# Optimization experiments

Measured on AMD Instinct MI355X. Metric: run time of the kernel, lower is better.

The kernel has to match this reference:

```python
import jax, jax.numpy as jnp
import numpy as np

B, L, D, H, HD = 4, 1024, 768, 12, 64

def setup_inputs() -> dict:
    key = jax.random.key(0)
    ks = jax.random.split(key, 8)
    s = 0.02
    return {
        "x": jax.random.normal(ks[0], (B, L, D), dtype=jnp.float32),
        "Wq": jax.random.normal(ks[1], (D, H * HD), dtype=jnp.float32) * s,
        "Wk": jax.random.normal(ks[2], (D, H * HD), dtype=jnp.float32) * s,
        "Wv": jax.random.normal(ks[3], (D, H * HD), dtype=jnp.float32) * s,
        "pre_attn": jax.random.normal(ks[4], (H, H), dtype=jnp.float32),
        "post_attn": jax.random.normal(ks[5], (H, H), dtype=jnp.float32),
        "Wo": jax.random.normal(ks[6], (H * HD, D), dtype=jnp.float32) * s,
        "bo": jnp.zeros((D,), dtype=jnp.float32),
    }

def reference(x, Wq, Wk, Wv, pre_attn, post_attn, Wo, bo):
    b, l, _ = x.shape
    # projections (no bias)
    q = x @ Wq  # [B, L, H*HD]
    k = x @ Wk
    v = x @ Wv
    # split heads: b l (h d) -> b h l d
    split = lambda t: t.reshape(b, l, H, HD).transpose(0, 2, 1, 3)
    qh, kh, vh = split(q), split(k), split(v)
    scale = 1.0 / jnp.sqrt(jnp.float32(HD))
    a = jnp.einsum('bhid,bhjd->bhij', qh, kh) * scale  # [B,H,L,L]
    # talking-heads: pre-softmax mix, softmax, post-softmax mix
    a = jnp.einsum('bhij,hg->bgij', a, pre_attn)
    a = jax.nn.softmax(a, axis=-1)
    a = jnp.einsum('bhij,hg->bgij', a, post_attn)
    av = jnp.einsum('bhij,bhjd->bhid', a, vh)  # [B,H,L,HD]
    # faithful to original: raw reshape of [(b h), l, d] -> [b, l, h*d]
    # (row-major, mixes h and l axes exactly like torch .reshape)
    av = av.reshape(b, l, H * HD)
    return av @ Wo + bo
```

## Files before the change

### kernel.cpp

```cpp
#include <hip/hip_runtime.h>

#define D_MODEL 768
#define NHEAD   12
#define HDIM    64
#define SEQ     1024
#define BATCH   4
#define QBLK    16
#define KVBLK   32

typedef __attribute__((ext_vector_type(8))) short short8v;
typedef __attribute__((ext_vector_type(4))) float f32x4;

__device__ __forceinline__ ushort f2bf(float f) {
    union { float f; unsigned u; } c; c.f = f;
    unsigned r = c.u + 0x7fffu + ((c.u >> 16) & 1u);
    return (ushort)(r >> 16);
}

__global__ void cast_bf16_kernel(const float* __restrict__ src,
                                 ushort* __restrict__ dst, int n4)
{
    int idx = blockIdx.x * blockDim.x + threadIdx.x;
    if (idx >= n4) return;
    float4 v = ((const float4*)src)[idx];
    ushort4 o;
    o.x = f2bf(v.x); o.y = f2bf(v.y); o.z = f2bf(v.z); o.w = f2bf(v.w);
    ((ushort4*)dst)[idx] = o;
}

__global__ __launch_bounds__(256) void castT_kernel(const float* __restrict__ W,
                                                    ushort* __restrict__ WT)
{
    __shared__ float tile[32][33];
    const int kb  = blockIdx.x * 32;
    const int nb  = blockIdx.y * 32;
    const int tid = threadIdx.x;
    const int r   = tid >> 3;
    const int c4  = (tid & 7) * 4;

    float4 v = *(const float4*)(W + (size_t)(kb + r) * 768 + nb + c4);
    tile[r][c4 + 0] = v.x; tile[r][c4 + 1] = v.y;
    tile[r][c4 + 2] = v.z; tile[r][c4 + 3] = v.w;
    __syncthreads();

    ushort4 o;
    o.x = f2bf(tile[c4 + 0][r]);
    o.y = f2bf(tile[c4 + 1][r]);
    o.z = f2bf(tile[c4 + 2][r]);
    o.w = f2bf(tile[c4 + 3][r]);
    *(ushort4*)(WT + (size_t)(nb + r) * 768 + kb + c4) = o;
}

__global__ __launch_bounds__(256) void vT_kernel(const ushort* __restrict__ vbf,
                                                 ushort* __restrict__ vt)
{
    __shared__ ushort tile[32][33];
    const int j0 = blockIdx.x * 32;
    const int d0 = blockIdx.y * 32;
    const int bh = blockIdx.z;
    const int b  = bh / NHEAD, h = bh % NHEAD;
    const int tid = threadIdx.x;
    const int r   = tid >> 3;
    const int c4  = (tid & 7) * 4;

    ushort4 v = *(const ushort4*)(vbf + ((size_t)b * SEQ + j0 + r) * D_MODEL + h * HDIM + d0 + c4);
    tile[r][c4 + 0] = v.x; tile[r][c4 + 1] = v.y;
    tile[r][c4 + 2] = v.z; tile[r][c4 + 3] = v.w;
    __syncthreads();

    ushort4 o;
    o.x = tile[c4 + 0][r]; o.y = tile[c4 + 1][r];
    o.z = tile[c4 + 2][r]; o.w = tile[c4 + 3][r];
    *(ushort4*)(vt + ((size_t)bh * HDIM + d0 + r) * SEQ + j0 + c4) = o;
}

template<int BF16OUT>
__global__ __launch_bounds__(256) void gemm_bf16_kernel(
    const ushort* __restrict__ A, const ushort* __restrict__ BT,
    void* __restrict__ C0v, void* __restrict__ C1v, void* __restrict__ C2v,
    const float* __restrict__ bias)
{
    __shared__ __align__(16) ushort As[128 * 32];
    __shared__ __align__(16) ushort Bs[128 * 32];

    const int bm  = blockIdx.x * 128;
    const int bnG = blockIdx.y * 128;
    const int sel = bnG / 768;
    void* Cv = (sel == 0) ? C0v : ((sel == 1) ? C1v : C2v);
    const int ncol0 = bnG - sel * 768;

    const int tid  = threadIdx.x;
    const int lane = tid & 63;
    const int wave = tid >> 6;
    const int wm = wave >> 1, wn = wave & 1;

    f32x4 acc[4][4];
    #pragma unroll
    for (int i = 0; i < 4; i++)
        #pragma unroll
        for (int j = 0; j < 4; j++)
            acc[i][j] = (f32x4){0.f, 0.f, 0.f, 0.f};

    const int sr = tid >> 2;
    const int sk = (tid & 3) * 8;
    const ushort* Ap = A  + (size_t)(bm  + sr) * 768 + sk;
    const ushort* Bp = BT + (size_t)(bnG + sr) * 768 + sk;
    char* AsDst = (char*)As + tid * 16;
    char* BsDst = (char*)Bs + tid * 16;

    for (int k0 = 0; k0 < 768; k0 += 32) {
        __syncthreads();
        __builtin_amdgcn_global_load_lds(
            (const __attribute__((address_space(1))) void*)(Ap + k0),
            (__attribute__((address_space(3))) void*)AsDst, 16, 0, 0);
        __builtin_amdgcn_global_load_lds(
            (const __attribute__((address_space(1))) void*)(Ap + (size_t)64 * 768 + k0),
            (__attribute__((address_space(3))) void*)(AsDst + 4096), 16, 0, 0);
        __builtin_amdgcn_global_load_lds(
            (const __attribute__((address_space(1))) void*)(Bp + k0),
            (__attribute__((address_space(3))) void*)BsDst, 16, 0, 0);
        __builtin_amdgcn_global_load_lds(
            (const __attribute__((address_space(1))) void*)(Bp + (size_t)64 * 768 + k0),
            (__attribute__((address_space(3))) void*)(BsDst + 4096), 16, 0, 0);
        __syncthreads();

        short8v a[4], b[4];
        #pragma unroll
        for (int i = 0; i < 4; i++)
            a[i] = *(const short8v*)((const char*)As +
                     (wm * 64 + i * 16 + (lane & 15)) * 64 + (lane >> 4) * 16);
        #pragma unroll
        for (int j = 0; j < 4; j++)
            b[j] = *(const short8v*)((const char*)Bs +
                     (wn * 64 + j * 16 + (lane & 15)) * 64 + (lane >> 4) * 16);
        #pragma unroll
        for (int i = 0; i < 4; i++)
            #pragma unroll
            for (int j = 0; j < 4; j++)
                acc[i][j] = __builtin_amdgcn_mfma_f32_16x16x32_bf16(a[i], b[j], acc[i][j], 0, 0, 0);
    }

    const int cc = lane & 15, cr = lane >> 4;
    #pragma unroll
    for (int j = 0; j < 4; j++) {
        const int col = ncol0 + wn * 64 + j * 16 + cc;
        const float badd = bias ? bias[col] : 0.f;
        #pragma unroll
        for (int i = 0; i < 4; i++) {
            #pragma unroll
            for (int r = 0; r < 4; r++) {
                const int row = bm + wm * 64 + i * 16 + cr * 4 + r;
                if (BF16OUT)
                    ((ushort*)Cv)[(size_t)row * 768 + col] = f2bf(acc[i][j][r] + badd);
                else
                    ((float*)Cv)[(size_t)row * 768 + col] = acc[i][j][r] + badd;
            }
        }
    }
}

__global__ __launch_bounds__(768, 1) void attn_mfma_kernel(
    const ushort* __restrict__ qb, const ushort* __restrict__ kb,
    const ushort* __restrict__ vt, const float* __restrict__ pre_attn,
    const float* __restrict__ post_attn, ushort* __restrict__ avb)
{
    __shared__ __align__(16) float s_raw[NHEAD][QBLK][36];
    __shared__ float pre_l[NHEAD * NHEAD];
    __shared__ float post_l[NHEAD * NHEAD];
    __shared__ float l_lds[NHEAD][QBLK];

    const int i0  = blockIdx.x * QBLK;
    const int b   = blockIdx.y;
    const int tid = threadIdx.x;
    const int lane = tid & 63;
    const int h    = tid >> 6;

    if (tid < 144) pre_l[tid] = pre_attn[tid] * 0.125f;
    else if (tid < 288) post_l[tid - 144] = post_attn[tid - 144];

    const int lr = lane & 15;
    const int lc = lane >> 4;

    const ushort* qbase = qb + ((size_t)b * SEQ + i0 + lr) * D_MODEL + h * HDIM + lc * 8;
    const short8v a_q0 = *(const short8v*)(qbase);
    const short8v a_q1 = *(const short8v*)(qbase + 32);

    const ushort* kbase  = kb + ((size_t)b * SEQ + lr) * D_MODEL + h * HDIM + lc * 8;
    const ushort* vtbase = vt + (((size_t)b * NHEAD + h) * HDIM + lr) * SEQ + lc * 8;

    float lsum = 0.f;
    for (int j0 = 0; j0 < SEQ; j0 += KVBLK) {
        f32x4 s_frag[2];
        #pragma unroll
        for (int cf = 0; cf < 2; cf++) {
            short8v bk0 = *(const short8v*)(kbase + (size_t)(j0 + cf * 16) * D_MODEL);
            short8v bk1 = *(const short8v*)(kbase + (size_t)(j0 + cf * 16) * D_MODEL + 32);
            f32x4 acc = (f32x4){0.f, 0.f, 0.f, 0.f};
            acc = __builtin_amdgcn_mfma_f32_16x16x32_bf16(a_q0, bk0, acc, 0, 0, 0);
            acc = __builtin_amdgcn_mfma_f32_16x16x32_bf16(a_q1, bk1, acc, 0, 0, 0);
            s_frag[cf] = acc;
        }
        __syncthreads();
        #pragma unroll
        for (int cf = 0; cf < 2; cf++)
            #pragma unroll
            for (int rr = 0; rr < 4; rr++)
                s_raw[h][lc * 4 + rr][cf * 16 + lr] = s_frag[cf][rr];
        __syncthreads();

        float mix[8];
        #pragma unroll
        for (int c = 0; c < 8; c++) mix[c] = 0.f;
        #pragma unroll
        for (int hh = 0; hh < NHEAD; hh++) {
            const float w = pre_l[hh * NHEAD + h];
            const float4 s0 = *(const float4*)(&s_raw[hh][lr][lc * 8]);
            const float4 s1 = *(const float4*)(&s_raw[hh][lr][lc * 8 + 4]);
            mix[0] = fmaf(s0.x, w, mix[0]); mix[1] = fmaf(s0.y, w, mix[1]);
            mix[2] = fmaf(s0.z, w, mix[2]); mix[3] = fmaf(s0.w, w, mix[3]);
            mix[4] = fmaf(s1.x, w, mix[4]); mix[5] = fmaf(s1.y, w, mix[5]);
            mix[6] = fmaf(s1.z, w, mix[6]); mix[7] = fmaf(s1.w, w, mix[7]);
        }
        #pragma unroll
        for (int c = 0; c < 8; c++) lsum += __expf(mix[c]);
    }
    float lrow = lsum;
    lrow += __shfl_xor(lrow, 16);
    lrow += __shfl_xor(lrow, 32);
    if (lc == 0) l_lds[h][lr] = lrow;
    __syncthreads();

    float il[NHEAD];
    #pragma unroll
    for (int hh = 0; hh < NHEAD; hh++) il[hh] = 1.f / l_lds[hh][lr];

    f32x4 o_acc[4];
    #pragma unroll
    for (int d = 0; d < 4; d++) o_acc[d] = (f32x4){0.f, 0.f, 0.f, 0.f};

    for (int j0 = 0; j0 < SEQ; j0 += KVBLK) {
        f32x4 s_frag[2];
        #pragma unroll
        for (int cf = 0; cf < 2; cf++) {
            short8v bk0 = *(const short8v*)(kbase + (size_t)(j0 + cf * 16) * D_MODEL);
            short8v bk1 = *(const short8v*)(kbase + (size_t)(j0 + cf * 16) * D_MODEL + 32);
            f32x4 acc = (f32x4){0.f, 0.f, 0.f, 0.f};
            acc = __builtin_amdgcn_mfma_f32_16x16x32_bf16(a_q0, bk0, acc, 0, 0, 0);
            acc = __builtin_amdgcn_mfma_f32_16x16x32_bf16(a_q1, bk1, acc, 0, 0, 0);
            s_frag[cf] = acc;
        }
        __syncthreads();
        #pragma unroll
        for (int cf = 0; cf < 2; cf++)
            #pragma unroll
            for (int rr = 0; rr < 4; rr++)
                s_raw[h][lc * 4 + rr][cf * 16 + lr] = s_frag[cf][rr];
        __syncthreads();

        float mix[8];
        #pragma unroll
        for (int c = 0; c < 8; c++) mix[c] = 0.f;
        #pragma unroll
        for (int hh = 0; hh < NHEAD; hh++) {
            const float w = pre_l[hh * NHEAD + h];
            const float4 s0 = *(const float4*)(&s_raw[hh][lr][lc * 8]);
            const float4 s1 = *(const float4*)(&s_raw[hh][lr][lc * 8 + 4]);
            mix[0] = fmaf(s0.x, w, mix[0]); mix[1] = fmaf(s0.y, w, mix[1]);
            mix[2] = fmaf(s0.z, w, mix[2]); mix[3] = fmaf(s0.w, w, mix[3]);
            mix[4] = fmaf(s1.x, w, mix[4]); mix[5] = fmaf(s1.y, w, mix[5]);
            mix[6] = fmaf(s1.z, w, mix[6]); mix[7] = fmaf(s1.w, w, mix[7]);
        }
        float e[8];
        #pragma unroll
        for (int c = 0; c < 8; c++) e[c] = __expf(mix[c]);

        __syncthreads();
        #pragma unroll
        for (int c = 0; c < 8; c += 4)
            *(float4*)(&s_raw[h][lr][lc * 8 + c]) = *(float4*)(&e[c]);
        __syncthreads();

        float pmix[8];
        #pragma unroll
        for (int c = 0; c < 8; c++) pmix[c] = 0.f;
        #pragma unroll
        for (int hh = 0; hh < NHEAD; hh++) {
            const float w = post_l[hh * NHEAD + h] * il[hh];
            const float4 e0 = *(const float4*)(&s_raw[hh][lr][lc * 8]);
            const float4 e1 = *(const float4*)(&s_raw[hh][lr][lc * 8 + 4]);
            pmix[0] = fmaf(e0.x, w, pmix[0]); pmix[1] = fmaf(e0.y, w, pmix[1]);
            pmix[2] = fmaf(e0.z, w, pmix[2]); pmix[3] = fmaf(e0.w, w, pmix[3]);
            pmix[4] = fmaf(e1.x, w, pmix[4]); pmix[5] = fmaf(e1.y, w, pmix[5]);
            pmix[6] = fmaf(e1.z, w, pmix[6]); pmix[7] = fmaf(e1.w, w, pmix[7]);
        }
        short8v pa;
        #pragma unroll
        for (int c = 0; c < 8; c++) ((ushort*)&pa)[c] = f2bf(pmix[c]);

        #pragma unroll
        for (int d = 0; d < 4; d++) {
            short8v bv = *(const short8v*)(vtbase + (size_t)(d * 16) * SEQ + j0);
            o_acc[d] = __builtin_amdgcn_mfma_f32_16x16x32_bf16(pa, bv, o_acc[d], 0, 0, 0);
        }
    }

    #pragma unroll
    for (int d = 0; d < 4; d++)
        #pragma unroll
        for (int rr = 0; rr < 4; rr++)
            avb[(((size_t)b * NHEAD + h) * SEQ + i0 + lc * 4 + rr) * HDIM + d * 16 + lr]
                = f2bf(o_acc[d][rr]);
}

extern "C" void kernel_launch(void* const* d_in, const int* in_sizes, int n_in,
                              void* d_out, int out_size, void* d_ws, size_t ws_size,
                              hipStream_t stream)
{
    const float* x    = (const float*)d_in[0];
    const float* Wq   = (const float*)d_in[1];
    const float* Wk   = (const float*)d_in[2];
    const float* Wv   = (const float*)d_in[3];
    const float* pre  = (const float*)d_in[4];
    const float* post = (const float*)d_in[5];
    const float* Wo   = (const float*)d_in[6];
    const float* bo   = (const float*)d_in[7];
    float* out = (float*)d_out;

    const size_t SZ = (size_t)BATCH * SEQ * D_MODEL;
    ushort* qbf    = (ushort*)d_ws;
    ushort* kbf    = qbf + SZ;
    ushort* vbf    = kbf + SZ;
    ushort* vt     = vbf + SZ;
    ushort* xb_avb = vt  + SZ;
    ushort* qkvT   = xb_avb + SZ;
    ushort* WoT    = qkvT + (size_t)2304 * 768;

    cast_bf16_kernel<<<(int)(SZ / 4 + 255) / 256, 256, 0, stream>>>(x, xb_avb, (int)(SZ / 4));
    castT_kernel<<<dim3(24, 24), 256, 0, stream>>>(Wq, qkvT);
    castT_kernel<<<dim3(24, 24), 256, 0, stream>>>(Wk, qkvT + (size_t)768 * 768);
    castT_kernel<<<dim3(24, 24), 256, 0, stream>>>(Wv, qkvT + (size_t)2 * 768 * 768);
    castT_kernel<<<dim3(24, 24), 256, 0, stream>>>(Wo, WoT);

    gemm_bf16_kernel<1><<<dim3(32, 18), 256, 0, stream>>>(xb_avb, qkvT, qbf, kbf, vbf, nullptr);

    vT_kernel<<<dim3(32, 2, BATCH * NHEAD), 256, 0, stream>>>(vbf, vt);

    attn_mfma_kernel<<<dim3(SEQ / QBLK, BATCH), 768, 0, stream>>>(qbf, kbf, vt, pre, post, xb_avb);

    gemm_bf16_kernel<0><<<dim3(32, 6), 256, 0, stream>>>(qbf == nullptr ? nullptr : xb_avb, WoT, out, out, out, bo);
}
```

Baseline: 355.1 us.

## Fuse V transpose into QKV GEMM, merge weight casts, double KV tile and buffers

The QKV GEMM epilogue now writes V directly in transposed per-head layout, which removes the separate vT kernel and the vbf buffer. The four weight cast-transpose launches are merged into one 3D-grid launch. In the attention kernel the KV block grows from 32 to 64 and the LDS score buffers are split or double-buffered, cutting __syncthreads per tile from four to one or two. exp is replaced by exp2 with log2e folded into the pre-mix weights. The cost is more LDS and registers per block, and the scattered ushort4 V-transpose stores may not coalesce well.

```diff
diff --git a/kernel.cpp b/kernel.cpp
--- a/kernel.cpp
+++ b/kernel.cpp
@@ -6,7 +6,8 @@
 #define SEQ     1024
 #define BATCH   4
 #define QBLK    16
-#define KVBLK   32
+#define KVBLK   64
+#define NT      (SEQ / KVBLK)
 
 typedef __attribute__((ext_vector_type(8))) short short8v;
 typedef __attribute__((ext_vector_type(4))) float f32x4;
@@ -28,10 +29,17 @@
     ((ushort4*)dst)[idx] = o;
 }
 
-__global__ __launch_bounds__(256) void castT_kernel(const float* __restrict__ W,
-                                                    ushort* __restrict__ WT)
+__global__ __launch_bounds__(256) void castT4_kernel(
+    const float* __restrict__ W0, const float* __restrict__ W1,
+    const float* __restrict__ W2, const float* __restrict__ W3,
+    ushort* __restrict__ D0, ushort* __restrict__ D1,
+    ushort* __restrict__ D2, ushort* __restrict__ D3)
 {
     __shared__ float tile[32][33];
+    const int z = blockIdx.z;
+    const float* W = (z == 0) ? W0 : (z == 1) ? W1 : (z == 2) ? W2 : W3;
+    ushort*     D = (z == 0) ? D0 : (z == 1) ? D1 : (z == 2) ? D2 : D3;
+
     const int kb  = blockIdx.x * 32;
     const int nb  = blockIdx.y * 32;
     const int tid = threadIdx.x;
@@ -48,37 +56,14 @@
     o.y = f2bf(tile[c4 + 1][r]);
     o.z = f2bf(tile[c4 + 2][r]);
     o.w = f2bf(tile[c4 + 3][r]);
-    *(ushort4*)(WT + (size_t)(nb + r) * 768 + kb + c4) = o;
-}
-
-__global__ __launch_bounds__(256) void vT_kernel(const ushort* __restrict__ vbf,
-                                                 ushort* __restrict__ vt)
-{
-    __shared__ ushort tile[32][33];
-    const int j0 = blockIdx.x * 32;
-    const int d0 = blockIdx.y * 32;
-    const int bh = blockIdx.z;
-    const int b  = bh / NHEAD, h = bh % NHEAD;
-    const int tid = threadIdx.x;
-    const int r   = tid >> 3;
-    const int c4  = (tid & 7) * 4;
-
-    ushort4 v = *(const ushort4*)(vbf + ((size_t)b * SEQ + j0 + r) * D_MODEL + h * HDIM + d0 + c4);
-    tile[r][c4 + 0] = v.x; tile[r][c4 + 1] = v.y;
-    tile[r][c4 + 2] = v.z; tile[r][c4 + 3] = v.w;
-    __syncthreads();
-
-    ushort4 o;
-    o.x = tile[c4 + 0][r]; o.y = tile[c4 + 1][r];
-    o.z = tile[c4 + 2][r]; o.w = tile[c4 + 3][r];
-    *(ushort4*)(vt + ((size_t)bh * HDIM + d0 + r) * SEQ + j0 + c4) = o;
+    *(ushort4*)(D + (size_t)(nb + r) * 768 + kb + c4) = o;
 }
 
 template<int BF16OUT>
 __global__ __launch_bounds__(256) void gemm_bf16_kernel(
     const ushort* __restrict__ A, const ushort* __restrict__ BT,
     void* __restrict__ C0v, void* __restrict__ C1v, void* __restrict__ C2v,
-    const float* __restrict__ bias)
+    const float* __restrict__ bias, ushort* __restrict__ VT)
 {
     __shared__ __align__(16) ushort As[128 * 32];
     __shared__ __align__(16) ushort Bs[128 * 32];
@@ -141,6 +126,23 @@
     }
 
     const int cc = lane & 15, cr = lane >> 4;
+    if (BF16OUT && VT != nullptr && sel == 2) {
+        #pragma unroll
+        for (int j = 0; j < 4; j++) {
+            const int hcol = ncol0 + wn * 64 + j * 16 + cc;
+            const int h2 = hcol >> 6, dd = hcol & 63;
+            #pragma unroll
+            for (int i = 0; i < 4; i++) {
+                const int row0 = bm + wm * 64 + i * 16 + cr * 4;
+                const int bb = row0 >> 10, jj = row0 & 1023;
+                ushort4 o;
+                o.x = f2bf(acc[i][j][0]); o.y = f2bf(acc[i][j][1]);
+                o.z = f2bf(acc[i][j][2]); o.w = f2bf(acc[i][j][3]);
+                *(ushort4*)(VT + (((size_t)bb * NHEAD + h2) * HDIM + dd) * SEQ + jj) = o;
+            }
+        }
+        return;
+    }
     #pragma unroll
     for (int j = 0; j < 4; j++) {
         const int col = ncol0 + wn * 64 + j * 16 + cc;
@@ -164,7 +166,8 @@
     const ushort* __restrict__ vt, const float* __restrict__ pre_attn,
     const float* __restrict__ post_attn, ushort* __restrict__ avb)
 {
-    __shared__ __align__(16) float s_raw[NHEAD][QBLK][36];
+    __shared__ __align__(16) float sA[NHEAD][QBLK][68];
+    __shared__ __align__(16) float sE[NHEAD][QBLK][68];
     __shared__ float pre_l[NHEAD * NHEAD];
     __shared__ float post_l[NHEAD * NHEAD];
     __shared__ float l_lds[NHEAD][QBLK];
@@ -175,7 +178,7 @@
     const int lane = tid & 63;
     const int h    = tid >> 6;
 
-    if (tid < 144) pre_l[tid] = pre_attn[tid] * 0.125f;
+    if (tid < 144) pre_l[tid] = pre_attn[tid] * (0.125f * 1.44269504f);
     else if (tid < 288) post_l[tid - 144] = post_attn[tid - 144];
 
     const int lr = lane & 15;
@@ -189,40 +192,50 @@
     const ushort* vtbase = vt + (((size_t)b * NHEAD + h) * HDIM + lr) * SEQ + lc * 8;
 
     float lsum = 0.f;
-    for (int j0 = 0; j0 < SEQ; j0 += KVBLK) {
-        f32x4 s_frag[2];
-        #pragma unroll
-        for (int cf = 0; cf < 2; cf++) {
-            short8v bk0 = *(const short8v*)(kbase + (size_t)(j0 + cf * 16) * D_MODEL);
-            short8v bk1 = *(const short8v*)(kbase + (size_t)(j0 + cf * 16) * D_MODEL + 32);
-            f32x4 acc = (f32x4){0.f, 0.f, 0.f, 0.f};
-            acc = __builtin_amdgcn_mfma_f32_16x16x32_bf16(a_q0, bk0, acc, 0, 0, 0);
-            acc = __builtin_amdgcn_mfma_f32_16x16x32_bf16(a_q1, bk1, acc, 0, 0, 0);
-            s_frag[cf] = acc;
-        }
-        __syncthreads();
-        #pragma unroll
-        for (int cf = 0; cf < 2; cf++)
+    for (int t = 0; t < NT; t++) {
+        const int j0 = t * KVBLK;
+        float (*S)[QBLK][68] = (t & 1) ? sE : sA;
+
+        f32x4 sf[4];
+        #pragma unroll
+        for (int cf = 0; cf < 4; cf++) {
+            const ushort* kp = kbase + (size_t)(j0 + cf * 16) * D_MODEL;
+            short8v bk0 = *(const short8v*)(kp);
+            short8v bk1 = *(const short8v*)(kp + 32);
+            f32x4 a = (f32x4){0.f, 0.f, 0.f, 0.f};
+            a = __builtin_amdgcn_mfma_f32_16x16x32_bf16(a_q0, bk0, a, 0, 0, 0);
+            a = __builtin_amdgcn_mfma_f32_16x16x32_bf16(a_q1, bk1, a, 0, 0, 0);
+            sf[cf] = a;
+        }
+        #pragma unroll
+        for (int cf = 0; cf < 4; cf++)
             #pragma unroll
             for (int rr = 0; rr < 4; rr++)
-                s_raw[h][lc * 4 + rr][cf * 16 + lr] = s_frag[cf][rr];
-        __syncthreads();
-
-        float mix[8];
-        #pragma unroll
-        for (int c = 0; c < 8; c++) mix[c] = 0.f;
+                S[h][lc * 4 + rr][cf * 16 + lr] = sf[cf][rr];
+        __syncthreads();
+
+        float mix[16];
+        #pragma unroll
+        for (int c = 0; c < 16; c++) mix[c] = 0.f;
         #pragma unroll
         for (int hh = 0; hh < NHEAD; hh++) {
             const float w = pre_l[hh * NHEAD + h];
-            const float4 s0 = *(const float4*)(&s_raw[hh][lr][lc * 8]);
-            const float4 s1 = *(const float4*)(&s_raw[hh][lr][lc * 8 + 4]);
-            mix[0] = fmaf(s0.x, w, mix[0]); mix[1] = fmaf(s0.y, w, mix[1]);
-            mix[2] = fmaf(s0.z, w, mix[2]); mix[3] = fmaf(s0.w, w, mix[3]);
-            mix[4] = fmaf(s1.x, w, mix[4]); mix[5] = fmaf(s1.y, w, mix[5]);
-            mix[6] = fmaf(s1.z, w, mix[6]); mix[7] = fmaf(s1.w, w, mix[7]);
-        }
-        #pragma unroll
-        for (int c = 0; c < 8; c++) lsum += __expf(mix[c]);
+            const float* row = &S[hh][lr][0];
+            const float4 a0 = *(const float4*)(row + lc * 8);
+            const float4 a1 = *(const float4*)(row + lc * 8 + 4);
+            const float4 a2 = *(const float4*)(row + 32 + lc * 8);
+            const float4 a3 = *(const float4*)(row + 36 + lc * 8);
+            mix[0]  = fmaf(a0.x, w, mix[0]);  mix[1]  = fmaf(a0.y, w, mix[1]);
+            mix[2]  = fmaf(a0.z, w, mix[2]);  mix[3]  = fmaf(a0.w, w, mix[3]);
+            mix[4]  = fmaf(a1.x, w, mix[4]);  mix[5]  = fmaf(a1.y, w, mix[5]);
+            mix[6]  = fmaf(a1.z, w, mix[6]);  mix[7]  = fmaf(a1.w, w, mix[7]);
+            mix[8]  = fmaf(a2.x, w, mix[8]);  mix[9]  = fmaf(a2.y, w, mix[9]);
+            mix[10] = fmaf(a2.z, w, mix[10]); mix[11] = fmaf(a2.w, w, mix[11]);
+            mix[12] = fmaf(a3.x, w, mix[12]); mix[13] = fmaf(a3.y, w, mix[13]);
+            mix[14] = fmaf(a3.z, w, mix[14]); mix[15] = fmaf(a3.w, w, mix[15]);
+        }
+        #pragma unroll
+        for (int c = 0; c < 16; c++) lsum += exp2f(mix[c]);
     }
     float lrow = lsum;
     lrow += __shfl_xor(lrow, 16);
@@ -238,69 +251,93 @@
     #pragma unroll
     for (int d = 0; d < 4; d++) o_acc[d] = (f32x4){0.f, 0.f, 0.f, 0.f};
 
-    for (int j0 = 0; j0 < SEQ; j0 += KVBLK) {
-        f32x4 s_frag[2];
-        #pragma unroll
-        for (int cf = 0; cf < 2; cf++) {
-            short8v bk0 = *(const short8v*)(kbase + (size_t)(j0 + cf * 16) * D_MODEL);
-            short8v bk1 = *(const short8v*)(kbase + (size_t)(j0 + cf * 16) * D_MODEL + 32);
-            f32x4 acc = (f32x4){0.f, 0.f, 0.f, 0.f};
-            acc = __builtin_amdgcn_mfma_f32_16x16x32_bf16(a_q0, bk0, acc, 0, 0, 0);
-            acc = __builtin_amdgcn_mfma_f32_16x16x32_bf16(a_q1, bk1, acc, 0, 0, 0);
-            s_frag[cf] = acc;
-        }
-        __syncthreads();
-        #pragma unroll
-        for (int cf = 0; cf < 2; cf++)
+    for (int t = 0; t < NT; t++) {
+        const int j0 = t * KVBLK;
+
+        f32x4 sf[4];
+        #pragma unroll
+        for (int cf = 0; cf < 4; cf++) {
+            const ushort* kp = kbase + (size_t)(j0 + cf * 16) * D_MODEL;
+            short8v bk0 = *(const short8v*)(kp);
+            short8v bk1 = *(const short8v*)(kp + 32);
+            f32x4 a = (f32x4){0.f, 0.f, 0.f, 0.f};
+            a = __builtin_amdgcn_mfma_f32_16x16x32_bf16(a_q0, bk0, a, 0, 0, 0);
+            a = __builtin_amdgcn_mfma_f32_16x16x32_bf16(a_q1, bk1, a, 0, 0, 0);
+            sf[cf] = a;
+        }
+        #pragma unroll
+        for (int cf = 0; cf < 4; cf++)
             #pragma unroll
             for (int rr = 0; rr < 4; rr++)
-                s_raw[h][lc * 4 + rr][cf * 16 + lr] = s_frag[cf][rr];
-        __syncthreads();
-
-        float mix[8];
-        #pragma unroll
-        for (int c = 0; c < 8; c++) mix[c] = 0.f;
+                sA[h][lc * 4 + rr][cf * 16 + lr] = sf[cf][rr];
+        __syncthreads();
+
+        float mix[16];
+        #pragma unroll
+        for (int c = 0; c < 16; c++) mix[c] = 0.f;
         #pragma unroll
         for (int hh = 0; hh < NHEAD; hh++) {
             const float w = pre_l[hh * NHEAD + h];
-            const float4 s0 = *(const float4*)(&s_raw[hh][lr][lc * 8]);
-            const float4 s1 = *(const float4*)(&s_raw[hh][lr][lc * 8 + 4]);
-            mix[0] = fmaf(s0.x, w, mix[0]); mix[1] = fmaf(s0.y, w, mix[1]);
-            mix[2] = fmaf(s0.z, w, mix[2]); mix[3] = fmaf(s0.w, w, mix[3]);
-            mix[4] = fmaf(s1.x, w, mix[4]); mix[5] = fmaf(s1.y, w, mix[5]);
-            mix[6] = fmaf(s1.z, w, mix[6]); mix[7] = fmaf(s1.w, w, mix[7]);
-        }
-        float e[8];
-        #pragma unroll
-        for (int c = 0; c < 8; c++) e[c] = __expf(mix[c]);
-
-        __syncthreads();
-        #pragma unroll
-        for (int c = 0; c < 8; c += 4)
-            *(float4*)(&s_raw[h][lr][lc * 8 + c]) = *(float4*)(&e[c]);
-        __syncthreads();
-
-        float pmix[8];
-        #pragma unroll
-        for (int c = 0; c < 8; c++) pmix[c] = 0.f;
+            const float* row = &sA[hh][lr][0];
+            const float4 a0 = *(const float4*)(row + lc * 8);
+            const float4 a1 = *(const float4*)(row + lc * 8 + 4);
+            const float4 a2 = *(const float4*)(row + 32 + lc * 8);
+            const float4 a3 = *(const float4*)(row + 36 + lc * 8);
+            mix[0]  = fmaf(a0.x, w, mix[0]);  mix[1]  = fmaf(a0.y, w, mix[1]);
+            mix[2]  = fmaf(a0.z, w, mix[2]);  mix[3]  = fmaf(a0.w, w, mix[3]);
+            mix[4]  = fmaf(a1.x, w, mix[4]);  mix[5]  = fmaf(a1.y, w, mix[5]);
+            mix[6]  = fmaf(a1.z, w, mix[6]);  mix[7]  = fmaf(a1.w, w, mix[7]);
+            mix[8]  = fmaf(a2.x, w, mix[8]);  mix[9]  = fmaf(a2.y, w, mix[9]);
+            mix[10] = fmaf(a2.z, w, mix[10]); mix[11] = fmaf(a2.w, w, mix[11]);
+            mix[12] = fmaf(a3.x, w, mix[12]); mix[13] = fmaf(a3.y, w, mix[13]);
+            mix[14] = fmaf(a3.z, w, mix[14]); mix[15] = fmaf(a3.w, w, mix[15]);
+        }
+        float e[16];
+        #pragma unroll
+        for (int c = 0; c < 16; c++) e[c] = exp2f(mix[c]);
+
+        {
+            float* row = &sE[h][lr][0];
+            *(float4*)(row + lc * 8)      = *(float4*)(&e[0]);
+            *(float4*)(row + lc * 8 + 4)  = *(float4*)(&e[4]);
+            *(float4*)(row + 32 + lc * 8) = *(float4*)(&e[8]);
+            *(float4*)(row + 36 + lc * 8) = *(float4*)(&e[12]);
+        }
+        __syncthreads();
+
+        float pm[16];
+        #pragma unroll
+        for (int c = 0; c < 16; c++) pm[c] = 0.f;
         #pragma unroll
         for (int hh = 0; hh < NHEAD; hh++) {
             const float w = post_l[hh * NHEAD + h] * il[hh];
-            const float4 e0 = *(const float4*)(&s_raw[hh][lr][lc * 8]);
-            const float4 e1 = *(const float4*)(&s_raw[hh][lr][lc * 8 + 4]);
-            pmix[0] = fmaf(e0.x, w, pmix[0]); pmix[1] = fmaf(e0.y, w, pmix[1]);
-            pmix[2] = fmaf(e0.z, w, pmix[2]); pmix[3] = fmaf(e0.w, w, pmix[3]);
-            pmix[4] = fmaf(e1.x, w, pmix[4]); pmix[5] = fmaf(e1.y, w, pmix[5]);
-            pmix[6] = fmaf(e1.z, w, pmix[6]); pmix[7] = fmaf(e1.w, w, pmix[7]);
-        }
-        short8v pa;
-        #pragma unroll
-        for (int c = 0; c < 8; c++) ((ushort*)&pa)[c] = f2bf(pmix[c]);
+            const float* row = &sE[hh][lr][0];
+            const float4 a0 = *(const float4*)(row + lc * 8);
+            const float4 a1 = *(const float4*)(row + lc * 8 + 4);
+            const float4 a2 = *(const float4*)(row + 32 + lc * 8);
+            const float4 a3 = *(const float4*)(row + 36 + lc * 8);
+            pm[0]  = fmaf(a0.x, w, pm[0]);  pm[1]  = fmaf(a0.y, w, pm[1]);
+            pm[2]  = fmaf(a0.z, w, pm[2]);  pm[3]  = fmaf(a0.w, w, pm[3]);
+            pm[4]  = fmaf(a1.x, w, pm[4]);  pm[5]  = fmaf(a1.y, w, pm[5]);
+            pm[6]  = fmaf(a1.z, w, pm[6]);  pm[7]  = fmaf(a1.w, w, pm[7]);
+            pm[8]  = fmaf(a2.x, w, pm[8]);  pm[9]  = fmaf(a2.y, w, pm[9]);
+            pm[10] = fmaf(a2.z, w, pm[10]); pm[11] = fmaf(a2.w, w, pm[11]);
+            pm[12] = fmaf(a3.x, w, pm[12]); pm[13] = fmaf(a3.y, w, pm[13]);
+            pm[14] = fmaf(a3.z, w, pm[14]); pm[15] = fmaf(a3.w, w, pm[15]);
+        }
+        short8v pa0, pa1;
+        #pragma unroll
+        for (int c = 0; c < 8; c++) {
+            ((ushort*)&pa0)[c] = f2bf(pm[c]);
+            ((ushort*)&pa1)[c] = f2bf(pm[8 + c]);
+        }
 
         #pragma unroll
         for (int d = 0; d < 4; d++) {
-            short8v bv = *(const short8v*)(vtbase + (size_t)(d * 16) * SEQ + j0);
-            o_acc[d] = __builtin_amdgcn_mfma_f32_16x16x32_bf16(pa, bv, o_acc[d], 0, 0, 0);
+            short8v bv0 = *(const short8v*)(vtbase + (size_t)(d * 16) * SEQ + j0);
+            short8v bv1 = *(const short8v*)(vtbase + (size_t)(d * 16) * SEQ + j0 + 32);
+            o_acc[d] = __builtin_amdgcn_mfma_f32_16x16x32_bf16(pa0, bv0, o_acc[d], 0, 0, 0);
+            o_acc[d] = __builtin_amdgcn_mfma_f32_16x16x32_bf16(pa1, bv1, o_acc[d], 0, 0, 0);
         }
     }
 
@@ -329,23 +366,22 @@
     const size_t SZ = (size_t)BATCH * SEQ * D_MODEL;
     ushort* qbf    = (ushort*)d_ws;
     ushort* kbf    = qbf + SZ;
-    ushort* vbf    = kbf + SZ;
-    ushort* vt     = vbf + SZ;
+    ushort* vt     = kbf + SZ;
     ushort* xb_avb = vt  + SZ;
     ushort* qkvT   = xb_avb + SZ;
     ushort* WoT    = qkvT + (size_t)2304 * 768;
 
     cast_bf16_kernel<<<(int)(SZ / 4 + 255) / 256, 256, 0, stream>>>(x, xb_avb, (int)(SZ / 4));
-    castT_kernel<<<dim3(24, 24), 256, 0, stream>>>(Wq, qkvT);
-    castT_kernel<<<dim3(24, 24), 256, 0, stream>>>(Wk, qkvT + (size_t)768 * 768);
-    castT_kernel<<<dim3(24, 24), 256, 0, stream>>>(Wv, qkvT + (size_t)2 * 768 * 768);
-    castT_kernel<<<dim3(24, 24), 256, 0, stream>>>(Wo, WoT);
-
-    gemm_bf16_kernel<1><<<dim3(32, 18), 256, 0, stream>>>(xb_avb, qkvT, qbf, kbf, vbf, nullptr);
-
-    vT_kernel<<<dim3(32, 2, BATCH * NHEAD), 256, 0, stream>>>(vbf, vt);
-
-    attn_mfma_kernel<<<dim3(SEQ / QBLK, BATCH), 768, 0, stream>>>(qbf, kbf, vt, pre, post, xb_avb);
-
-    gemm_bf16_kernel<0><<<dim3(32, 6), 256, 0, stream>>>(qbf == nullptr ? nullptr : xb_avb, WoT, out, out, out, bo);
-}
+    castT4_kernel<<<dim3(24, 24, 4), 256, 0, stream>>>(
+        Wq, Wk, Wv, Wo,
+        qkvT, qkvT + (size_t)768 * 768, qkvT + (size_t)2 * 768 * 768, WoT);
+
+    gemm_bf16_kernel<1><<<dim3(32, 18), 256, 0, stream>>>(
+        xb_avb, qkvT, qbf, kbf, nullptr, nullptr, vt);
+
+    attn_mfma_kernel<<<dim3(SEQ / QBLK, BATCH), 768, 0, stream>>>(
+        qbf, kbf, vt, pre, post, xb_avb);
+
+    gemm_bf16_kernel<0><<<dim3(32, 6), 256, 0, stream>>>(
+        xb_avb, WoT, out, out, out, bo, nullptr);
+}
```

Measured after the change: 377.1 us. +6.2%, slower.
